# Kernel optimization log

Hardware: AMD Instinct MI355X
Metric: run time of the kernel (lower is better)

## Reference

```python
import jax, jax.numpy as jnp
import numpy as np

C_CURV = 0.001
L = 10
N = 16
OMEGA = 1.0
EPS = 1e-6


def _fnmap(x, a0, a, b):
    # x: [M, C]; radial Fourier gate
    r = jnp.maximum(jnp.linalg.norm(x, axis=1, keepdims=True), EPS)  # [M,1]
    n = jnp.arange(1, N + 1, dtype=x.dtype)[None, :]                 # [1,N]
    angle = OMEGA * (r * n)                                          # [M,N]
    f_r = a0 + jnp.cos(angle) @ a[:, None] + jnp.sin(angle) @ b[:, None]  # [M,1]
    return f_r * x


def _log_map_origin(x, c):
    sc = jnp.sqrt(c)
    rn = jnp.maximum(jnp.linalg.norm(x, axis=1, keepdims=True), EPS)
    arg = jnp.minimum(sc * rn, 1.0 - 1e-5)
    return (jnp.arctanh(arg) / (sc * rn)) * x


def _exp_map_origin(v, c):
    sc = jnp.sqrt(c)
    rn = jnp.maximum(jnp.linalg.norm(v, axis=1, keepdims=True), EPS)
    return (jnp.tanh(sc * rn) / (sc * rn)) * v


def setup_inputs() -> dict:
    key = jax.random.key(0)
    ks = jax.random.split(key, 8)
    B, C, H, W = 32, 256, 64, 64
    x = jax.random.normal(ks[0], (B, C, H, W), dtype=jnp.float32) * 0.1
    inp = {
        "x": x,
        "a0_1": jnp.ones((1,), jnp.float32),
        "a_1": jax.random.normal(ks[1], (N,), jnp.float32) * 0.02,
        "b_1": jax.random.normal(ks[2], (N,), jnp.float32) * 0.02,
        "a0_2": jnp.ones((1,), jnp.float32),
        "a_2": jax.random.normal(ks[3], (N,), jnp.float32) * 0.02,
        "b_2": jax.random.normal(ks[4], (N,), jnp.float32) * 0.02,
        "phi": jax.random.normal(ks[5], (C,), jnp.float32) * 0.02,
        "alpha": jnp.ones((1,), jnp.float32),
        "beta": jnp.zeros((1,), jnp.float32),
    }
    return inp


def reference(x, a0_1, a_1, b_1, a0_2, a_2, b_2, phi, alpha, beta):
    B, C, H, W = x.shape
    h0 = jnp.transpose(x, (0, 2, 3, 1)).reshape(-1, C)  # [B*H*W, C]
    u = _log_map_origin(h0, C_CURV)
    u1 = _fnmap(u, a0_1, a_1, b_1)
    U = jnp.fft.rfft(u1, axis=1)                         # [M, C//2+1]
    ang = L * phi
    Hf = jax.lax.complex(jnp.cos(ang), jnp.sin(ang))     # [C]
    V = U * Hf[None, : U.shape[-1]]
    v0 = jnp.fft.irfft(V, n=C, axis=1)
    v1 = _fnmap(v0, a0_2, a_2, b_2)
    y = _exp_map_origin(v1, C_CURV)
    out = alpha * y + beta * h0
    return jnp.transpose(out.reshape(B, H, W, C), (0, 3, 1, 2))
```

## Files before the change

kernel.cpp:

```cpp
#include <hip/hip_runtime.h>
#include <math.h>

typedef __attribute__((ext_vector_type(8))) unsigned short ushort8;
typedef __attribute__((ext_vector_type(8))) __bf16 bf16x8;
typedef __attribute__((ext_vector_type(4))) float f32x4;

constexpr int   CDIM  = 256;
constexpr int   HWSP  = 4096;
constexpr int   PPB   = 64;
constexpr float SQRTC = 0.031622776601683794f;
constexpr float EPSR  = 1e-6f;

__device__ inline unsigned short f2bf(float x) {
    unsigned int u = __float_as_uint(x);
    u += 0x7FFFu + ((u >> 16) & 1u);
    return (unsigned short)(u >> 16);
}
__device__ inline int swz(int pos) { return ((pos ^ (pos >> 2)) & 15) << 3; }

__global__ void build_wpk(const float* __restrict__ phi,
                          unsigned short* __restrict__ wpk) {
    __shared__ float w[256];
    const int d = threadIdx.x;
    {
        const float step = 6.283185307179586f / 256.0f;
        double s = 0.0;
        for (int k = 1; k <= 127; ++k) {
            int kd = (k * d) & 255;
            s += 2.0 * (double)cosf(10.0f * phi[k] + step * (float)kd);
        }
        s += (double)cosf(10.0f * phi[0]);
        double c128 = (double)cosf(10.0f * phi[128]);
        s += (d & 1) ? -c128 : c128;
        w[d] = (float)(s * (1.0 / 256.0));
    }
    __syncthreads();
    const int l = d & 63, q = d >> 6;
    for (int blk = q; blk < 128; blk += 4) {
        const int outc = (blk & 15) * 16 + (l & 15);
        const int ch0  = (blk >> 4) * 32 + (l >> 4) * 8;
        ushort8 u;
        #pragma unroll
        for (int j = 0; j < 8; ++j)
            u[j] = f2bf(w[(outc - (ch0 + j)) & 255]);
        *reinterpret_cast<ushort8*>(&wpk[(size_t)(blk * 64 + l) * 8]) = u;
    }
}

__device__ inline float fourier_gate(float r, float A0,
                                     const float* __restrict__ a,
                                     const float* __restrict__ b) {
    float sn, cs;
    sincosf(r, &sn, &cs);
    float c = cs, s = sn, f = A0;
    #pragma unroll
    for (int n = 0; n < 16; ++n) {
        f = fmaf(a[n], c, f);
        f = fmaf(b[n], s, f);
        float c2 = fmaf(c, cs, -s * sn);
        float s2 = fmaf(s, cs,  c * sn);
        c = c2; s = s2;
    }
    return f;
}

__global__ __launch_bounds__(256, 4)
void fused_mfma(const float* __restrict__ x,
                const float* __restrict__ a0_1, const float* __restrict__ a1,
                const float* __restrict__ b1,
                const float* __restrict__ a0_2, const float* __restrict__ a2,
                const float* __restrict__ b2,
                const float* __restrict__ phi,
                const float* __restrict__ alpha, const float* __restrict__ beta,
                const unsigned short* __restrict__ wpk,
                float* __restrict__ out) {
    __shared__ __align__(16) unsigned short Xl[PPB][CDIM];
    __shared__ __align__(16) float stats[3][4][PPB];
    __shared__ __align__(16) float sobuf[PPB];

    {
        const unsigned bid = blockIdx.x;
        const int h = (bid ^ (bid >> 3) ^ (bid >> 7)) & 7;
        for (int i = 0; i < h; ++i) __builtin_amdgcn_s_sleep(32);
    }

    const int t  = threadIdx.x;
    const int l  = t & 63;
    const int g  = t >> 6;
    const int lr = l & 15;
    const int lk = l >> 4;
    const int b  = blockIdx.x >> 6;
    const int s0 = (blockIdx.x & 63) * PPB;
    const float* xb = x + (size_t)b * CDIM * HWSP + s0;

    f32x4 vns = {0.f,0.f,0.f,0.f}, vs0 = {0.f,0.f,0.f,0.f}, vsa = {0.f,0.f,0.f,0.f};
    const int posq = t & 15;
    #pragma unroll
    for (int i = 0; i < 2; ++i) {
        const int co = i * 16 + (t >> 4);
        f32x4 v[8];
        #pragma unroll
        for (int j = 0; j < 8; ++j)
            v[j] = *reinterpret_cast<const f32x4*>(
                       &xb[(size_t)(co * 8 + j) * HWSP + posq * 4]);
        #pragma unroll
        for (int j = 0; j < 8; ++j) {
            vns += v[j] * v[j];
            vs0 += v[j];
            vsa  = (j & 1) ? vsa - v[j] : vsa + v[j];
        }
        #pragma unroll
        for (int r = 0; r < 4; ++r) {
            ushort8 u;
            #pragma unroll
            for (int j = 0; j < 8; ++j) u[j] = f2bf(v[j][r]);
            const int pos = posq * 4 + r;
            *reinterpret_cast<ushort8*>(&Xl[pos][(co * 8) ^ swz(pos)]) = u;
        }
    }
    #pragma unroll
    for (int r = 0; r < 4; ++r) {
        float aa = vns[r], ss = vs0[r], mm = vsa[r];
        aa += __shfl_xor(aa, 16, 64); aa += __shfl_xor(aa, 32, 64);
        ss += __shfl_xor(ss, 16, 64); ss += __shfl_xor(ss, 32, 64);
        mm += __shfl_xor(mm, 16, 64); mm += __shfl_xor(mm, 32, 64);
        vns[r] = aa; vs0[r] = ss; vsa[r] = mm;
    }
    if (lk == 0) {
        *reinterpret_cast<f32x4*>(&stats[0][g][posq * 4]) = vns;
        *reinterpret_cast<f32x4*>(&stats[1][g][posq * 4]) = vs0;
        *reinterpret_cast<f32x4*>(&stats[2][g][posq * 4]) = vsa;
    }
    __syncthreads();

    if (t < PPB) {
        float nsq = stats[0][0][t] + stats[0][1][t] + stats[0][2][t] + stats[0][3][t];
        float S0  = stats[1][0][t] + stats[1][1][t] + stats[1][2][t] + stats[1][3][t];
        float Sa  = stats[2][0][t] + stats[2][1][t] + stats[2][2][t] + stats[2][3][t];
        float sin0 = sinf(10.0f * phi[0]);
        float sinN = sinf(10.0f * phi[128]);
        float n0  = sqrtf(nsq);
        float rn0 = fmaxf(n0, EPSR);
        float arg = fminf(SQRTC * rn0, 1.0f - 1e-5f);
        float ls  = atanhf(arg) / (SQRTC * rn0);
        float r1  = fmaxf(ls * n0, EPSR);
        float s1  = ls * fourier_gate(r1, a0_1[0], a1, b1);
        float dn2 = fmaxf(nsq - (S0 * S0 * sin0 * sin0 + Sa * Sa * sinN * sinN)
                                 * (1.0f / 256.0f), 0.f);
        float nv  = sqrtf(dn2) * fabsf(s1);
        float r2  = fmaxf(nv, EPSR);
        float f2  = fourier_gate(r2, a0_2[0], a2, b2);
        float rn1 = fmaxf(fabsf(f2) * nv, EPSR);
        float es  = tanhf(SQRTC * rn1) / (SQRTC * rn1);
        sobuf[t]  = alpha[0] * es * f2 * s1;
    }

    f32x4 acc[4][4];
    #pragma unroll
    for (int m = 0; m < 4; ++m)
        #pragma unroll
        for (int n = 0; n < 4; ++n)
            acc[m][n] = f32x4{0.f, 0.f, 0.f, 0.f};

    #pragma unroll
    for (int ks = 0; ks < 8; ++ks) {
        const int kb = ks * 32 + lk * 8;
        bf16x8 af[4], bw[4];
        #pragma unroll
        for (int m = 0; m < 4; ++m) {
            const int pos = m * 16 + lr;
            af[m] = __builtin_bit_cast(bf16x8,
                *reinterpret_cast<const ushort8*>(&Xl[pos][kb ^ swz(pos)]));
        }
        #pragma unroll
        for (int n = 0; n < 4; ++n)
            bw[n] = __builtin_bit_cast(bf16x8,
                *reinterpret_cast<const ushort8*>(
                    &wpk[(size_t)((ks * 16 + g * 4 + n) * 64 + l) * 8]));
        #pragma unroll
        for (int m = 0; m < 4; ++m)
            #pragma unroll
            for (int n = 0; n < 4; ++n)
                acc[m][n] = __builtin_amdgcn_mfma_f32_16x16x32_bf16(
                    af[m], bw[n], acc[m][n], 0, 0, 0);
    }
    __syncthreads();

    const float bb = beta[0];
    float* ob = out + (size_t)b * CDIM * HWSP + s0;
    if (bb == 0.f) {
        #pragma unroll
        for (int m = 0; m < 4; ++m) {
            const int p0 = m * 16 + lk * 4;
            const f32x4 sob = *reinterpret_cast<const f32x4*>(&sobuf[p0]);
            #pragma unroll
            for (int n = 0; n < 4; ++n) {
                const int outc = (g * 4 + n) * 16 + lr;
                f32x4 vv = acc[m][n] * sob;
                *reinterpret_cast<f32x4*>(&ob[(size_t)outc * HWSP + p0]) = vv;
            }
        }
    } else {
        #pragma unroll
        for (int m = 0; m < 4; ++m) {
            const int p0 = m * 16 + lk * 4;
            const f32x4 sob = *reinterpret_cast<const f32x4*>(&sobuf[p0]);
            #pragma unroll
            for (int n = 0; n < 4; ++n) {
                const int outc = (g * 4 + n) * 16 + lr;
                const f32x4 xv = *reinterpret_cast<const f32x4*>(
                                     &xb[(size_t)outc * HWSP + p0]);
                f32x4 vv = acc[m][n] * sob + bb * xv;
                *reinterpret_cast<f32x4*>(&ob[(size_t)outc * HWSP + p0]) = vv;
            }
        }
    }
}

extern "C" void kernel_launch(void* const* d_in, const int* in_sizes, int n_in,
                              void* d_out, int out_size, void* d_ws, size_t ws_size,
                              hipStream_t stream) {
    const float* x     = (const float*)d_in[0];
    const float* a0_1  = (const float*)d_in[1];
    const float* a1    = (const float*)d_in[2];
    const float* b1    = (const float*)d_in[3];
    const float* a0_2  = (const float*)d_in[4];
    const float* a2    = (const float*)d_in[5];
    const float* b2    = (const float*)d_in[6];
    const float* phi   = (const float*)d_in[7];
    const float* alpha = (const float*)d_in[8];
    const float* beta  = (const float*)d_in[9];

    unsigned short* wpk = (unsigned short*)d_ws;

    build_wpk<<<1, 256, 0, stream>>>(phi, wpk);

    const int B = in_sizes[0] / (CDIM * HWSP);
    fused_mfma<<<dim3(B * (HWSP / PPB)), dim3(256), 0, stream>>>(
        x, a0_1, a1, b1, a0_2, a2, b2, phi, alpha, beta, wpk, (float*)d_out);
}
```

Measured before the change: 83.97 us.

## Stage compact circulant weight table in LDS instead of packed global weights

Replaces the fully packed 256x256 bf16 circulant weight matrix with a compact table of 8 shifted copies of the 256-tap filter (768 entries each), which every block copies into shared memory. B-operand fragments are then read from LDS at shifted offsets rather than streamed from global/L2 for each k-step. The staggered s_sleep start-up delay is also removed. This adds about 12KB of LDS per block, which may lower occupancy, and adds a small prologue copy.

```diff
diff --git a/kernel.cpp b/kernel.cpp
--- a/kernel.cpp
+++ b/kernel.cpp
@@ -8,6 +8,7 @@
 constexpr int   CDIM  = 256;
 constexpr int   HWSP  = 4096;
 constexpr int   PPB   = 64;
+constexpr int   TLEN  = 768;
 constexpr float SQRTC = 0.031622776601683794f;
 constexpr float EPSR  = 1e-6f;
 
@@ -18,8 +19,8 @@
 }
 __device__ inline int swz(int pos) { return ((pos ^ (pos >> 2)) & 15) << 3; }
 
-__global__ void build_wpk(const float* __restrict__ phi,
-                          unsigned short* __restrict__ wpk) {
+__global__ void build_wtab(const float* __restrict__ phi,
+                           unsigned short* __restrict__ Tg) {
     __shared__ float w[256];
     const int d = threadIdx.x;
     {
@@ -35,15 +36,9 @@
         w[d] = (float)(s * (1.0 / 256.0));
     }
     __syncthreads();
-    const int l = d & 63, q = d >> 6;
-    for (int blk = q; blk < 128; blk += 4) {
-        const int outc = (blk & 15) * 16 + (l & 15);
-        const int ch0  = (blk >> 4) * 32 + (l >> 4) * 8;
-        ushort8 u;
-        #pragma unroll
-        for (int j = 0; j < 8; ++j)
-            u[j] = f2bf(w[(outc - (ch0 + j)) & 255]);
-        *reinterpret_cast<ushort8*>(&wpk[(size_t)(blk * 64 + l) * 8]) = u;
+    for (int idx = d; idx < 8 * TLEN; idx += 256) {
+        const int s = idx / TLEN, i = idx - s * TLEN;
+        Tg[idx] = f2bf(w[(512 - i - s) & 255]);
     }
 }
 
@@ -72,17 +67,12 @@
                 const float* __restrict__ b2,
                 const float* __restrict__ phi,
                 const float* __restrict__ alpha, const float* __restrict__ beta,
-                const unsigned short* __restrict__ wpk,
+                const unsigned short* __restrict__ Tg,
                 float* __restrict__ out) {
     __shared__ __align__(16) unsigned short Xl[PPB][CDIM];
+    __shared__ __align__(16) unsigned short Tsh[8 * TLEN];
     __shared__ __align__(16) float stats[3][4][PPB];
     __shared__ __align__(16) float sobuf[PPB];
-
-    {
-        const unsigned bid = blockIdx.x;
-        const int h = (bid ^ (bid >> 3) ^ (bid >> 7)) & 7;
-        for (int i = 0; i < h; ++i) __builtin_amdgcn_s_sleep(32);
-    }
 
     const int t  = threadIdx.x;
     const int l  = t & 63;
@@ -92,6 +82,13 @@
     const int b  = blockIdx.x >> 6;
     const int s0 = (blockIdx.x & 63) * PPB;
     const float* xb = x + (size_t)b * CDIM * HWSP + s0;
+
+    #pragma unroll
+    for (int i = 0; i < 3; ++i) {
+        const int c8 = t + i * 256;
+        *reinterpret_cast<ushort8*>(&Tsh[c8 * 8]) =
+            *reinterpret_cast<const ushort8*>(&Tg[c8 * 8]);
+    }
 
     f32x4 vns = {0.f,0.f,0.f,0.f}, vs0 = {0.f,0.f,0.f,0.f}, vsa = {0.f,0.f,0.f,0.f};
     const int posq = t & 15;
@@ -155,6 +152,7 @@
         sobuf[t]  = alpha[0] * es * f2 * s1;
     }
 
+    const int so767 = ((-lr) & 7) * (TLEN - 1);
     f32x4 acc[4][4];
     #pragma unroll
     for (int m = 0; m < 4; ++m)
@@ -173,10 +171,11 @@
                 *reinterpret_cast<const ushort8*>(&Xl[pos][kb ^ swz(pos)]));
         }
         #pragma unroll
-        for (int n = 0; n < 4; ++n)
+        for (int n = 0; n < 4; ++n) {
+            const int base = kb + 512 - ((g * 4 + n) * 16 + lr);
             bw[n] = __builtin_bit_cast(bf16x8,
-                *reinterpret_cast<const ushort8*>(
-                    &wpk[(size_t)((ks * 16 + g * 4 + n) * 64 + l) * 8]));
+                *reinterpret_cast<const ushort8*>(&Tsh[base + so767]));
+        }
         #pragma unroll
         for (int m = 0; m < 4; ++m)
             #pragma unroll
@@ -231,11 +230,11 @@
     const float* alpha = (const float*)d_in[8];
     const float* beta  = (const float*)d_in[9];
 
-    unsigned short* wpk = (unsigned short*)d_ws;
-
-    build_wpk<<<1, 256, 0, stream>>>(phi, wpk);
+    unsigned short* Tg = (unsigned short*)d_ws;
+
+    build_wtab<<<1, 256, 0, stream>>>(phi, Tg);
 
     const int B = in_sizes[0] / (CDIM * HWSP);
     fused_mfma<<<dim3(B * (HWSP / PPB)), dim3(256), 0, stream>>>(
-        x, a0_1, a1, b1, a0_2, a2, b2, phi, alpha, beta, wpk, (float*)d_out);
-}
+        x, a0_1, a1, b1, a0_2, a2, b2, phi, alpha, beta, Tg, (float*)d_out);
+}
```

Result: no change. 84.42 us (+0.5%).
